# Performance work log

Hardware: AMD Instinct MI355X
Metric: run time of the kernel (lower is better)

## Reference

```python
import jax, jax.numpy as jnp
import numpy as np

N_LAYERS = 4
D_IN = 64
D_OUT = 64
D_MODEL = 512
D_STATE = 256
RMIN, RMAX, MAX_PHASE = 0.8, 0.95, 2.0 * np.pi


def setup_inputs() -> dict:
    key = jax.random.key(0)
    rng = np.random.default_rng(0)
    B, L = 8, 2048
    u = jax.random.normal(key, (B, L, D_IN), dtype=jnp.float32)
    # encoder/decoder (nn.Linear, bias=False): weight shape [out, in]
    encoder_w = jnp.asarray(rng.standard_normal((D_MODEL, D_IN)) / np.sqrt(D_IN), jnp.float32)
    decoder_w = jnp.asarray(rng.standard_normal((D_OUT, D_MODEL)) / np.sqrt(D_MODEL), jnp.float32)
    # LRU params per block (standard ring init on eigenvalues)
    u1 = rng.uniform(size=(N_LAYERS, D_STATE))
    u2 = rng.uniform(size=(N_LAYERS, D_STATE))
    nu_log = jnp.asarray(np.log(-0.5 * np.log(u1 * (RMAX**2 - RMIN**2) + RMIN**2)), jnp.float32)
    theta_log = jnp.asarray(np.log(MAX_PHASE * u2), jnp.float32)
    B_re = jnp.asarray(rng.standard_normal((N_LAYERS, D_STATE, D_MODEL)) / np.sqrt(2 * D_MODEL), jnp.float32)
    B_im = jnp.asarray(rng.standard_normal((N_LAYERS, D_STATE, D_MODEL)) / np.sqrt(2 * D_MODEL), jnp.float32)
    C_re = jnp.asarray(rng.standard_normal((N_LAYERS, D_MODEL, D_STATE)) / np.sqrt(D_STATE), jnp.float32)
    C_im = jnp.asarray(rng.standard_normal((N_LAYERS, D_MODEL, D_STATE)) / np.sqrt(D_STATE), jnp.float32)
    D = jnp.asarray(rng.standard_normal((N_LAYERS, D_MODEL)), jnp.float32)
    # GLU feedforward: y = (x W1^T) * sigmoid(x W2^T)
    W1 = jnp.asarray(rng.standard_normal((N_LAYERS, D_MODEL, D_MODEL)) / np.sqrt(D_MODEL), jnp.float32)
    W2 = jnp.asarray(rng.standard_normal((N_LAYERS, D_MODEL, D_MODEL)) / np.sqrt(D_MODEL), jnp.float32)
    res_logit = jnp.full((N_LAYERS,), -1.0, jnp.float32)
    return dict(u=u, encoder_w=encoder_w, decoder_w=decoder_w, nu_log=nu_log,
                theta_log=theta_log, B_re=B_re, B_im=B_im, C_re=C_re, C_im=C_im,
                D=D, W1=W1, W2=W2, res_logit=res_logit)


def _lru(x, nu, th, Bre, Bim, Cre, Cim, Dv):
    # diagonal complex LRU: h_t = lam*h_{t-1} + gamma*B u_t ; y = Re(C h) + D*u
    lam = jnp.exp(-jnp.exp(nu) + 1j * jnp.exp(th)).astype(jnp.complex64)  # [N]
    gam = jnp.sqrt(1.0 - jnp.abs(lam) ** 2).astype(jnp.complex64)
    Bc = (Bre + 1j * Bim).astype(jnp.complex64)  # [N, D]
    Bu = jnp.einsum('bld,nd->bln', x.astype(jnp.complex64), Bc) * gam  # [B,L,N]
    lam_b = jnp.broadcast_to(lam, Bu.shape)

    def comb(a, b):
        return (a[0] * b[0], a[1] * b[0] + b[1])

    _, h = jax.lax.associative_scan(comb, (lam_b, Bu), axis=1)
    Cc = (Cre + 1j * Cim).astype(jnp.complex64)  # [D, N]
    return jnp.real(jnp.einsum('bln,dn->bld', h, Cc)) + Dv * x


def reference(u, encoder_w, decoder_w, nu_log, theta_log, B_re, B_im, C_re, C_im, D, W1, W2, res_logit):
    x = jnp.einsum('bli,mi->blm', u, encoder_w)  # encoder
    for k in range(N_LAYERS):
        z = _lru(x, nu_log[k], theta_log[k], B_re[k], B_im[k], C_re[k], C_im[k], D[k])
        z = jnp.einsum('bld,od->blo', z, W1[k]) * jax.nn.sigmoid(jnp.einsum('bld,od->blo', z, W2[k]))
        x = x + jax.nn.sigmoid(res_logit[k]) * z  # gated residual (dropout=0)
    return jnp.einsum('blm,om->blo', x, decoder_w)  # decoder
```

## Files before the change

### kernel.cpp

```cpp
#include <hip/hip_runtime.h>
#include <cmath>

#define DM 512
#define DS 256
#define NL 4
#define BATCH 8
#define SEQ 2048
#define MROWS (BATCH*SEQ)
#define LCH 32
#define NCH 64

typedef unsigned short ushort_t;
typedef unsigned int uint_t;
typedef __attribute__((ext_vector_type(8))) short short8;
typedef __attribute__((ext_vector_type(4))) float floatx4;

__device__ __forceinline__ float sigmoidf_(float v) { return 1.0f / (1.0f + __expf(-v)); }

__device__ __forceinline__ ushort_t f2bf(float f) {
    union { float f; unsigned int u; } c; c.f = f;
    unsigned int u = c.u;
    u += 0x7fffu + ((u >> 16) & 1u);
    return (ushort_t)(u >> 16);
}
__device__ __forceinline__ float bf2f(uint_t h) {
    union { unsigned int u; float f; } c; c.u = (h & 0xffffu) << 16; return c.f;
}
__device__ __forceinline__ uint_t pack2(float a, float b) {
    return (uint_t)f2bf(a) | ((uint_t)f2bf(b) << 16);
}

#define AS1 __attribute__((address_space(1)))
#define AS3 __attribute__((address_space(3)))
__device__ __forceinline__ void gl_lds16(const void* g, void* l) {
    __builtin_amdgcn_global_load_lds((const AS1 uint_t*)g, (AS3 uint_t*)l, 16, 0, 0);
}

struct GemmArgs {
    const ushort_t* A;
    const ushort_t* Wa;
    const ushort_t* Wb;
    const ushort_t* xbf_in;
    const float* gam;
    const float* Dv;
    float* of32;
    ushort_t* obf;
    const float* resp;
    int K;
    int N;
    int layer;
};

#define PREFETCH_TILE(it_, buf_)                                                        \
    do {                                                                                \
        const size_t kb_ = (size_t)(it_) * 64;                                          \
        char* dst_ = smem + (buf_) * HALF;                                              \
        gl_lds16(Ap + (size_t)(wid * 16 + lrow) * Kb + kb_, dst_ + wid * 1024);         \
        gl_lds16(Ap + (size_t)((wid + 4) * 16 + lrow) * Kb + kb_,                       \
                 dst_ + (wid + 4) * 1024);                                              \
        gl_lds16(B0p + (size_t)(wid * 16 + lrow) * Kb + kb_, dst_ + AB + wid * 1024);   \
        if constexpr (BN == 128) {                                                      \
            gl_lds16(B0p + (size_t)((wid + 4) * 16 + lrow) * Kb + kb_,                  \
                     dst_ + AB + (wid + 4) * 1024);                                     \
        }                                                                               \
        if constexpr (DUAL) {                                                           \
            gl_lds16(B1p + (size_t)(wid * 16 + lrow) * Kb + kb_,                        \
                     dst_ + AB + BB + wid * 1024);                                      \
            if constexpr (BN == 128) {                                                  \
                gl_lds16(B1p + (size_t)((wid + 4) * 16 + lrow) * Kb + kb_,              \
                         dst_ + AB + BB + (wid + 4) * 1024);                            \
            }                                                                           \
        }                                                                               \
    } while (0)

template<int BN, int EPI, int DUAL>
__launch_bounds__(256, DUAL ? 2 : 3)
__global__ void mgemm(const GemmArgs p) {
    constexpr int BM = 128;
    constexpr int MT = (BN == 128) ? 4 : 2;
    constexpr int NT = 4;
    constexpr int WROWS = MT * 16;
    constexpr int AB = 8192;
    constexpr int BB = (BN == 128) ? 8192 : 4096;
    constexpr int B1B = DUAL ? BB : 0;
    constexpr int HALF = AB + BB + B1B;
    constexpr int EPB = (EPI == 4) ? 0 : 32 * 132 * 4;
    constexpr int SMB = (2 * HALF > EPB) ? 2 * HALF : EPB;
    __shared__ __align__(16) char smem[SMB];

    const int K = p.K, N = p.N;
    const int tid = threadIdx.x, lane = tid & 63, wid = tid >> 6;
    const int wm = (BN == 128) ? (wid & 1) : wid;
    const int wn = (BN == 128) ? (wid >> 1) : 0;
    const int m0 = blockIdx.x * BM, n0 = blockIdx.y * BN;
    const int q = lane >> 4, r16 = lane & 15;
    const int lrow = lane >> 2;
    const size_t Kb = (size_t)K * 2;
    const char* Ap  = (const char*)p.A  + (size_t)m0 * Kb + (lane & 3) * 16;
    const char* B0p = (const char*)p.Wa + (size_t)n0 * Kb + (lane & 3) * 16;
    const char* B1p = (const char*)p.Wb + (size_t)n0 * Kb + (lane & 3) * 16;

    floatx4 acc0[MT][NT] = {};
    floatx4 acc1[DUAL ? MT : 1][DUAL ? NT : 1] = {};

    const int iters = K >> 5;
    PREFETCH_TILE(0, 0);
    for (int it = 0; it < iters; ++it) {
        __syncthreads();
        if (it + 1 < iters) PREFETCH_TILE(it + 1, (it + 1) & 1);
        const ushort_t* As  = (const ushort_t*)(smem + (it & 1) * HALF);
        const ushort_t* Bs0 = (const ushort_t*)(smem + (it & 1) * HALF + AB);
        const ushort_t* Bs1 = (const ushort_t*)(smem + (it & 1) * HALF + AB + BB);

        short8 af[MT], b0[NT], b1[DUAL ? NT : 1];
#pragma unroll
        for (int i = 0; i < MT; ++i)
            af[i] = *(const short8*)&As[(wm * WROWS + i * 16 + r16) * 32 + q * 8];
#pragma unroll
        for (int j = 0; j < NT; ++j) {
            b0[j] = *(const short8*)&Bs0[(wn * 64 + j * 16 + r16) * 32 + q * 8];
            if constexpr (DUAL)
                b1[j] = *(const short8*)&Bs1[(wn * 64 + j * 16 + r16) * 32 + q * 8];
        }
#pragma unroll
        for (int i = 0; i < MT; ++i)
#pragma unroll
            for (int j = 0; j < NT; ++j) {
                acc0[i][j] = __builtin_amdgcn_mfma_f32_16x16x32_bf16(af[i], b0[j], acc0[i][j], 0, 0, 0);
                if constexpr (DUAL)
                    acc1[i][j] = __builtin_amdgcn_mfma_f32_16x16x32_bf16(af[i], b1[j], acc1[i][j], 0, 0, 0);
            }
    }

    if constexpr (EPI == 4) {
#pragma unroll
        for (int i = 0; i < MT; ++i)
#pragma unroll
            for (int j = 0; j < NT; ++j)
#pragma unroll
                for (int rr = 0; rr < 4; ++rr) {
                    const int row = m0 + wm * WROWS + i * 16 + q * 4 + rr;
                    const int col = wn * 64 + j * 16 + r16;
                    p.of32[(size_t)row * N + col] = acc0[i][j][rr];
                }
        return;
    } else {
        float* eps = (float*)smem;
        float rsv = 0.f;
        if constexpr (EPI == 3) rsv = sigmoidf_(p.resp[p.layer]);

#pragma unroll
        for (int i = 0; i < MT; ++i) {
            __syncthreads();
#pragma unroll
            for (int j = 0; j < NT; ++j) {
                const int colt = wn * 64 + j * 16 + r16;
#pragma unroll
                for (int rr = 0; rr < 4; ++rr) {
                    float v = acc0[i][j][rr];
                    if constexpr (EPI == 1) v *= p.gam[(n0 + colt) >> 1];
                    if constexpr (EPI == 3) v = rsv * v * sigmoidf_(acc1[i][j][rr]);
                    eps[(wm * 16 + q * 4 + rr) * 132 + colt] = v;
                }
            }
            __syncthreads();
            const int row_r = tid >> 3, colg = (tid & 7) * 16;
            const int grow = m0 + (row_r >> 4) * 64 + i * 16 + (row_r & 15);
            const int gcol = n0 + colg;
            float4 f[4];
#pragma unroll
            for (int c = 0; c < 4; ++c) f[c] = *(float4*)&eps[row_r * 132 + colg + c * 4];
            const size_t ob = (size_t)grow * N + gcol;

            if constexpr (EPI == 2) {
                uint_t xp[8];
                *(uint4*)(xp)     = *(const uint4*)(p.xbf_in + ob);
                *(uint4*)(xp + 4) = *(const uint4*)(p.xbf_in + ob + 8);
#pragma unroll
                for (int c = 0; c < 4; ++c) {
                    float4 dv = *(const float4*)(p.Dv + gcol + c * 4);
                    f[c].x += dv.x * bf2f(xp[2 * c]);
                    f[c].y += dv.y * bf2f(xp[2 * c] >> 16);
                    f[c].z += dv.z * bf2f(xp[2 * c + 1]);
                    f[c].w += dv.w * bf2f(xp[2 * c + 1] >> 16);
                }
            } else if constexpr (EPI == 3) {
                uint_t xp[8];
                *(uint4*)(xp)     = *(const uint4*)(p.xbf_in + ob);
                *(uint4*)(xp + 4) = *(const uint4*)(p.xbf_in + ob + 8);
#pragma unroll
                for (int c = 0; c < 4; ++c) {
                    f[c].x += bf2f(xp[2 * c]);
                    f[c].y += bf2f(xp[2 * c] >> 16);
                    f[c].z += bf2f(xp[2 * c + 1]);
                    f[c].w += bf2f(xp[2 * c + 1] >> 16);
                }
            }
            uint4 p0, p1;
            p0.x = pack2(f[0].x, f[0].y); p0.y = pack2(f[0].z, f[0].w);
            p0.z = pack2(f[1].x, f[1].y); p0.w = pack2(f[1].z, f[1].w);
            p1.x = pack2(f[2].x, f[2].y); p1.y = pack2(f[2].z, f[2].w);
            p1.z = pack2(f[3].x, f[3].y); p1.w = pack2(f[3].z, f[3].w);
            *(uint4*)(p.obf + ob) = p0;
            *(uint4*)(p.obf + ob + 8) = p1;
        }
    }
}

__global__ void prep_all(const float* __restrict__ u, const float* __restrict__ enc,
                         const float* __restrict__ dec, const float* __restrict__ nu,
                         const float* __restrict__ th,
                         const float* __restrict__ Bre, const float* __restrict__ Bim,
                         const float* __restrict__ Cre, const float* __restrict__ Cim,
                         const float* __restrict__ W1, const float* __restrict__ W2,
                         ushort_t* __restrict__ WBb, ushort_t* __restrict__ Wzb,
                         ushort_t* __restrict__ W1b, ushort_t* __restrict__ W2b,
                         ushort_t* __restrict__ encb, ushort_t* __restrict__ decb,
                         ushort_t* __restrict__ ubf,
                         float* __restrict__ lre, float* __restrict__ lim,
                         float* __restrict__ gm) {
    const int idx = blockIdx.x * 256 + threadIdx.x;
    const int k = idx & 511, n = (idx >> 9) & 511, l = idx >> 18;
    {
        const int s = n >> 1, part = n & 1;
        const float* src = part ? Bim : Bre;
        WBb[idx] = f2bf(src[((size_t)l * DS + s) * DM + k]);
    }
    {
        const int s = k >> 1, part = k & 1;
        float v = part ? -Cim[((size_t)l * DM + n) * DS + s]
                       :  Cre[((size_t)l * DM + n) * DS + s];
        Wzb[idx] = f2bf(v);
    }
    W1b[idx] = f2bf(W1[idx]);
    W2b[idx] = f2bf(W2[idx]);
    ubf[idx] = f2bf(u[idx]);
    if (idx < DM * 64) { encb[idx] = f2bf(enc[idx]); decb[idx] = f2bf(dec[idx]); }
    if (idx < NL * DS) {
        float a = expf(-expf(nu[idx])), t = expf(th[idx]);
        lre[idx] = a * cosf(t);
        lim[idx] = a * sinf(t);
        gm[idx] = sqrtf(fmaxf(0.f, 1.f - a * a));
    }
}

__global__ void scan_ends(const uint_t* __restrict__ Bu, const float* __restrict__ lre_,
                          const float* __restrict__ lim_, float* __restrict__ carry) {
    const int s = threadIdx.x;
    const int blk = blockIdx.x, b = blk >> 6, c = blk & 63;
    const float lre = lre_[s], lim = lim_[s];
    float hre = 0.f, him = 0.f;
    size_t base = ((size_t)b * SEQ + (size_t)c * LCH) * DS + s;
#pragma unroll 8
    for (int i = 0; i < LCH; ++i, base += DS) {
        uint_t u = Bu[base];
        float br = bf2f(u), bi = bf2f(u >> 16);
        float nr = fmaf(lre, hre, fmaf(-lim, him, br));
        float ni = fmaf(lre, him, fmaf(lim, hre, bi));
        hre = nr; him = ni;
    }
    carry[(size_t)blk * 512 + s] = hre;
    carry[(size_t)blk * 512 + DS + s] = him;
}

__global__ void scan_carry(float* __restrict__ carry, const float* __restrict__ lre_,
                           const float* __restrict__ lim_) {
    const int s = threadIdx.x, b = blockIdx.x;
    float pre = lre_[s], pim = lim_[s];
    for (int t = 0; t < 5; ++t) {
        float nr = pre * pre - pim * pim, ni = 2.f * pre * pim;
        pre = nr; pim = ni;
    }
    size_t base = (size_t)b * NCH * 512 + s;
    float gre = carry[base], gim = carry[base + DS];
    for (int c = 1; c < NCH; ++c) {
        size_t id = base + (size_t)c * 512;
        float cr = carry[id], ci = carry[id + DS];
        float nr = fmaf(pre, gre, fmaf(-pim, gim, cr));
        float ni = fmaf(pre, gim, fmaf(pim, gre, ci));
        gre = nr; gim = ni;
        carry[id] = gre; carry[id + DS] = gim;
    }
}

__global__ void scan_apply(const uint_t* __restrict__ Bu, const float* __restrict__ lre_,
                           const float* __restrict__ lim_, const float* __restrict__ carry,
                           uint_t* __restrict__ h) {
    const int s = threadIdx.x;
    const int blk = blockIdx.x, b = blk >> 6, c = blk & 63;
    const float lre = lre_[s], lim = lim_[s];
    float hre = 0.f, him = 0.f;
    if (c > 0) {
        size_t cb = (size_t)(blk - 1) * 512 + s;
        hre = carry[cb]; him = carry[cb + DS];
    }
    size_t base = ((size_t)b * SEQ + (size_t)c * LCH) * DS + s;
#pragma unroll 8
    for (int i = 0; i < LCH; ++i, base += DS) {
        uint_t u = Bu[base];
        float br = bf2f(u), bi = bf2f(u >> 16);
        float nr = fmaf(lre, hre, fmaf(-lim, him, br));
        float ni = fmaf(lre, him, fmaf(lim, hre, bi));
        hre = nr; him = ni;
        h[base] = pack2(hre, him);
    }
}

extern "C" void kernel_launch(void* const* d_in, const int* in_sizes, int n_in,
                              void* d_out, int out_size, void* d_ws, size_t ws_size,
                              hipStream_t stream) {
    const float* u   = (const float*)d_in[0];
    const float* enc = (const float*)d_in[1];
    const float* dec = (const float*)d_in[2];
    const float* nu  = (const float*)d_in[3];
    const float* th  = (const float*)d_in[4];
    const float* Bre = (const float*)d_in[5];
    const float* Bim = (const float*)d_in[6];
    const float* Cre = (const float*)d_in[7];
    const float* Cim = (const float*)d_in[8];
    const float* Dp  = (const float*)d_in[9];
    const float* W1  = (const float*)d_in[10];
    const float* W2  = (const float*)d_in[11];
    const float* res = (const float*)d_in[12];
    float* out = (float*)d_out;

    const size_t MD = (size_t)MROWS * DM;
    float* carry = (float*)d_ws;
    float* lre  = carry + (size_t)BATCH * NCH * 512;
    float* lim  = lre + NL * DS;
    float* gmt  = lim + NL * DS;
    ushort_t* xbf  = (ushort_t*)(gmt + NL * DS);
    ushort_t* Bubf = xbf + MD;
    ushort_t* hbf  = Bubf + MD;
    ushort_t* zbf  = hbf + MD;
    ushort_t* ubf  = zbf;
    ushort_t* WBb  = zbf + MD;
    ushort_t* Wzb  = WBb + (size_t)NL * DM * DM;
    ushort_t* W1b  = Wzb + (size_t)NL * DM * DM;
    ushort_t* W2b  = W1b + (size_t)NL * DM * DM;
    ushort_t* encb = W2b + (size_t)NL * DM * DM;
    ushort_t* decb = encb + DM * 64;

    prep_all<<<NL * DM * DM / 256, 256, 0, stream>>>(
        u, enc, dec, nu, th, Bre, Bim, Cre, Cim, W1, W2,
        WBb, Wzb, W1b, W2b, encb, decb, ubf, lre, lim, gmt);

    const dim3 gFull(MROWS / 128, DM / 128);

    {
        GemmArgs a = {};
        a.A = ubf; a.Wa = encb; a.K = 64; a.N = DM;
        a.obf = xbf;
        mgemm<128, 0, 0><<<gFull, 256, 0, stream>>>(a);
    }

    for (int k = 0; k < NL; ++k) {
        {
            GemmArgs a = {};
            a.A = xbf; a.Wa = WBb + (size_t)k * DM * DM; a.K = DM; a.N = DM;
            a.obf = Bubf; a.gam = gmt + k * DS;
            mgemm<128, 1, 0><<<gFull, 256, 0, stream>>>(a);
        }
        scan_ends<<<BATCH * NCH, 256, 0, stream>>>((const uint_t*)Bubf,
                                                   lre + k * DS, lim + k * DS, carry);
        scan_carry<<<BATCH, 256, 0, stream>>>(carry, lre + k * DS, lim + k * DS);
        scan_apply<<<BATCH * NCH, 256, 0, stream>>>((const uint_t*)Bubf,
                                                    lre + k * DS, lim + k * DS, carry,
                                                    (uint_t*)hbf);
        {
            GemmArgs a = {};
            a.A = hbf; a.Wa = Wzb + (size_t)k * DM * DM; a.K = DM; a.N = DM;
            a.obf = zbf; a.xbf_in = xbf; a.Dv = Dp + k * DM;
            mgemm<128, 2, 0><<<gFull, 256, 0, stream>>>(a);
        }
        {
            GemmArgs a = {};
            a.A = zbf; a.Wa = W1b + (size_t)k * DM * DM; a.Wb = W2b + (size_t)k * DM * DM;
            a.K = DM; a.N = DM;
            a.obf = xbf; a.xbf_in = xbf; a.resp = res; a.layer = k;
            mgemm<128, 3, 1><<<gFull, 256, 0, stream>>>(a);
        }
    }
    {
        GemmArgs a = {};
        a.A = xbf; a.Wa = decb; a.K = DM; a.N = 64;
        a.of32 = out;
        mgemm<64, 4, 0><<<dim3(MROWS / 128, 1), 256, 0, stream>>>(a);
    }
}
```

Before: 373.9 us.

## Fuse three-pass chunked scan into single-pass kernel with decoupled lookback

Replaces the scan_ends / scan_carry / scan_apply sequence with one kernel. Each block takes a ticket-ordered virtual block id, scans its chunk into registers, publishes its chunk-end state, and sets a per-batch bitmask flag. It then spin-waits on up to twelve preceding chunks and combines their end states with powers of lambda to get its prefix, which assumes contributions from farther chunks are negligible. This removes a second read of Bu, two kernel launches and the serial carry pass, in exchange for spin-wait synchronisation, higher register use and a truncated lookback approximation.

After: 764.2 us. 2.04x slower.

```diff
diff --git a/kernel.cpp b/kernel.cpp
--- a/kernel.cpp
+++ b/kernel.cpp
@@ -12,6 +12,7 @@
 
 typedef unsigned short ushort_t;
 typedef unsigned int uint_t;
+typedef unsigned long long ull_t;
 typedef __attribute__((ext_vector_type(8))) short short8;
 typedef __attribute__((ext_vector_type(4))) float floatx4;
 
@@ -218,7 +219,8 @@
                          ushort_t* __restrict__ encb, ushort_t* __restrict__ decb,
                          ushort_t* __restrict__ ubf,
                          float* __restrict__ lre, float* __restrict__ lim,
-                         float* __restrict__ gm) {
+                         float* __restrict__ gm,
+                         ull_t* __restrict__ msk, int* __restrict__ tkt) {
     const int idx = blockIdx.x * 256 + threadIdx.x;
     const int k = idx & 511, n = (idx >> 9) & 511, l = idx >> 18;
     {
@@ -242,68 +244,80 @@
         lim[idx] = a * sinf(t);
         gm[idx] = sqrtf(fmaxf(0.f, 1.f - a * a));
     }
-}
-
-__global__ void scan_ends(const uint_t* __restrict__ Bu, const float* __restrict__ lre_,
-                          const float* __restrict__ lim_, float* __restrict__ carry) {
+    if (idx < NL * BATCH) msk[idx] = 0ull;
+    if (idx < NL) tkt[idx] = 0;
+}
+
+__global__ __launch_bounds__(256) void scan_fused(
+        const uint_t* __restrict__ Bu, const float* __restrict__ lre_,
+        const float* __restrict__ lim_, float* __restrict__ carry,
+        ull_t* __restrict__ msk, int* __restrict__ tkt,
+        uint_t* __restrict__ h) {
+    __shared__ int vblk_s;
+    if (threadIdx.x == 0) vblk_s = atomicAdd(tkt, 1);
+    __syncthreads();
+    const int blk = vblk_s;
     const int s = threadIdx.x;
-    const int blk = blockIdx.x, b = blk >> 6, c = blk & 63;
+    const int b = blk >> 6, c = blk & 63;
     const float lre = lre_[s], lim = lim_[s];
-    float hre = 0.f, him = 0.f;
-    size_t base = ((size_t)b * SEQ + (size_t)c * LCH) * DS + s;
-#pragma unroll 8
-    for (int i = 0; i < LCH; ++i, base += DS) {
-        uint_t u = Bu[base];
-        float br = bf2f(u), bi = bf2f(u >> 16);
-        float nr = fmaf(lre, hre, fmaf(-lim, him, br));
-        float ni = fmaf(lre, him, fmaf(lim, hre, bi));
-        hre = nr; him = ni;
-    }
-    carry[(size_t)blk * 512 + s] = hre;
-    carry[(size_t)blk * 512 + DS + s] = him;
-}
-
-__global__ void scan_carry(float* __restrict__ carry, const float* __restrict__ lre_,
-                           const float* __restrict__ lim_) {
-    const int s = threadIdx.x, b = blockIdx.x;
-    float pre = lre_[s], pim = lim_[s];
-    for (int t = 0; t < 5; ++t) {
-        float nr = pre * pre - pim * pim, ni = 2.f * pre * pim;
-        pre = nr; pim = ni;
-    }
-    size_t base = (size_t)b * NCH * 512 + s;
-    float gre = carry[base], gim = carry[base + DS];
-    for (int c = 1; c < NCH; ++c) {
-        size_t id = base + (size_t)c * 512;
-        float cr = carry[id], ci = carry[id + DS];
-        float nr = fmaf(pre, gre, fmaf(-pim, gim, cr));
-        float ni = fmaf(pre, gim, fmaf(pim, gre, ci));
-        gre = nr; gim = ni;
-        carry[id] = gre; carry[id + DS] = gim;
-    }
-}
-
-__global__ void scan_apply(const uint_t* __restrict__ Bu, const float* __restrict__ lre_,
-                           const float* __restrict__ lim_, const float* __restrict__ carry,
-                           uint_t* __restrict__ h) {
-    const int s = threadIdx.x;
-    const int blk = blockIdx.x, b = blk >> 6, c = blk & 63;
-    const float lre = lre_[s], lim = lim_[s];
-    float hre = 0.f, him = 0.f;
+
+    float hre[LCH], him[LCH];
+    float xr = 0.f, xi = 0.f;
+    const size_t base = ((size_t)b * SEQ + (size_t)c * LCH) * DS + s;
+#pragma unroll
+    for (int i = 0; i < LCH; ++i) {
+        uint_t uu = Bu[base + (size_t)i * DS];
+        float br = bf2f(uu), bi = bf2f(uu >> 16);
+        float nr = fmaf(lre, xr, fmaf(-lim, xi, br));
+        float ni = fmaf(lre, xi, fmaf(lim, xr, bi));
+        xr = nr; xi = ni;
+        hre[i] = nr; him[i] = ni;
+    }
+
+    const size_t cb = (size_t)blk * 512 + s;
+    carry[cb] = xr; carry[cb + DS] = xi;
+    __syncthreads();
+    if (threadIdx.x == 0) {
+        __threadfence();
+        __hip_atomic_fetch_or(&msk[b], 1ull << c, __ATOMIC_RELEASE, __HIP_MEMORY_SCOPE_AGENT);
+    }
+
     if (c > 0) {
-        size_t cb = (size_t)(blk - 1) * 512 + s;
-        hre = carry[cb]; him = carry[cb + DS];
-    }
-    size_t base = ((size_t)b * SEQ + (size_t)c * LCH) * DS + s;
-#pragma unroll 8
-    for (int i = 0; i < LCH; ++i, base += DS) {
-        uint_t u = Bu[base];
-        float br = bf2f(u), bi = bf2f(u >> 16);
-        float nr = fmaf(lre, hre, fmaf(-lim, him, br));
-        float ni = fmaf(lre, him, fmaf(lim, hre, bi));
-        hre = nr; him = ni;
-        h[base] = pack2(hre, him);
-    }
+        float pre = lre, pim = lim;
+#pragma unroll
+        for (int t = 0; t < 5; ++t) {
+            float nr = pre * pre - pim * pim, ni = 2.f * pre * pim;
+            pre = nr; pim = ni;
+        }
+        const int depth = (c < 12) ? c : 12;
+        const ull_t need = ((1ull << depth) - 1ull) << (c - depth);
+        while ((__hip_atomic_load(&msk[b], __ATOMIC_ACQUIRE, __HIP_MEMORY_SCOPE_AGENT)
+                & need) != need) {
+            __builtin_amdgcn_s_sleep(2);
+        }
+        float gre = 0.f, gim = 0.f, pwr = 1.f, pwi = 0.f;
+        for (int j = c - 1; j >= c - depth; --j) {
+            const size_t jb = (size_t)(b * NCH + j) * 512 + s;
+            float er = carry[jb], ei = carry[jb + DS];
+            gre = fmaf(pwr, er, fmaf(-pwi, ei, gre));
+            gim = fmaf(pwr, ei, fmaf(pwi, er, gim));
+            float nr = pwr * pre - pwi * pim, ni = pwr * pim + pwi * pre;
+            pwr = nr; pwi = ni;
+        }
+        float pr = fmaf(lre, gre, -lim * gim);
+        float pi = fmaf(lre, gim,  lim * gre);
+#pragma unroll
+        for (int i = 0; i < LCH; ++i) {
+            hre[i] += pr; him[i] += pi;
+            float nr = fmaf(lre, pr, -lim * pi);
+            float ni = fmaf(lre, pi,  lim * pr);
+            pr = nr; pi = ni;
+        }
+    }
+
+#pragma unroll
+    for (int i = 0; i < LCH; ++i)
+        h[base + (size_t)i * DS] = pack2(hre[i], him[i]);
 }
 
 extern "C" void kernel_launch(void* const* d_in, const int* in_sizes, int n_in,
@@ -329,7 +343,9 @@
     float* lre  = carry + (size_t)BATCH * NCH * 512;
     float* lim  = lre + NL * DS;
     float* gmt  = lim + NL * DS;
-    ushort_t* xbf  = (ushort_t*)(gmt + NL * DS);
+    ull_t* msk  = (ull_t*)(gmt + NL * DS);
+    int*   tkt  = (int*)(msk + NL * BATCH);
+    ushort_t* xbf  = (ushort_t*)(tkt + NL);
     ushort_t* Bubf = xbf + MD;
     ushort_t* hbf  = Bubf + MD;
     ushort_t* zbf  = hbf + MD;
@@ -343,7 +359,7 @@
 
     prep_all<<<NL * DM * DM / 256, 256, 0, stream>>>(
         u, enc, dec, nu, th, Bre, Bim, Cre, Cim, W1, W2,
-        WBb, Wzb, W1b, W2b, encb, decb, ubf, lre, lim, gmt);
+        WBb, Wzb, W1b, W2b, encb, decb, ubf, lre, lim, gmt, msk, tkt);
 
     const dim3 gFull(MROWS / 128, DM / 128);
 
@@ -361,12 +377,9 @@
             a.obf = Bubf; a.gam = gmt + k * DS;
             mgemm<128, 1, 0><<<gFull, 256, 0, stream>>>(a);
         }
-        scan_ends<<<BATCH * NCH, 256, 0, stream>>>((const uint_t*)Bubf,
-                                                   lre + k * DS, lim + k * DS, carry);
-        scan_carry<<<BATCH, 256, 0, stream>>>(carry, lre + k * DS, lim + k * DS);
-        scan_apply<<<BATCH * NCH, 256, 0, stream>>>((const uint_t*)Bubf,
-                                                    lre + k * DS, lim + k * DS, carry,
-                                                    (uint_t*)hbf);
+        scan_fused<<<BATCH * NCH, 256, 0, stream>>>(
+            (const uint_t*)Bubf, lre + k * DS, lim + k * DS, carry,
+            msk + (size_t)k * BATCH, tkt + k, (uint_t*)hbf);
         {
             GemmArgs a = {};
             a.A = hbf; a.Wa = Wzb + (size_t)k * DM * DM; a.K = DM; a.N = DM;
```

## Replace serial scan carry kernel with truncated lookback and remap GEMM blocks per XCD

Applied to the files above, without the earlier changes.

Drops the scan_carry kernel, which walks the 64 chunk carries one after another with only 8 blocks. Instead, each scan_apply block builds its incoming state from up to 12 preceding chunk end-states, weighted by powers of lambda^32. This removes a launch and a serial, low-occupancy pass, at the cost of a small truncation error that depends on |lambda| staying bounded below 1 (it is at most 0.95 by construction). Separately, the GEMM remaps block indices so that blocks sharing an XCD handle contiguous M tiles, which is meant to improve L2 reuse. The remap hardcodes a grid width of 128.

After: 388.5 us. +3.9%, slower.

```diff
diff --git a/kernel.cpp b/kernel.cpp
--- a/kernel.cpp
+++ b/kernel.cpp
@@ -92,7 +92,13 @@
     const int tid = threadIdx.x, lane = tid & 63, wid = tid >> 6;
     const int wm = (BN == 128) ? (wid & 1) : wid;
     const int wn = (BN == 128) ? (wid >> 1) : 0;
-    const int m0 = blockIdx.x * BM, n0 = blockIdx.y * BN;
+
+    const int flat = blockIdx.y * 128 + blockIdx.x;
+    const int xcd = flat & 7, sidx = flat >> 3;
+    const int bx = xcd * 16 + (sidx & 15);
+    const int by = sidx >> 4;
+
+    const int m0 = bx * BM, n0 = by * BN;
     const int q = lane >> 4, r16 = lane & 15;
     const int lrow = lane >> 2;
     const size_t Kb = (size_t)K * 2;
@@ -244,8 +250,9 @@
     }
 }
 
-__global__ void scan_ends(const uint_t* __restrict__ Bu, const float* __restrict__ lre_,
-                          const float* __restrict__ lim_, float* __restrict__ carry) {
+__global__ __launch_bounds__(256) void scan_ends(
+        const uint_t* __restrict__ Bu, const float* __restrict__ lre_,
+        const float* __restrict__ lim_, float* __restrict__ carry) {
     const int s = threadIdx.x;
     const int blk = blockIdx.x, b = blk >> 6, c = blk & 63;
     const float lre = lre_[s], lim = lim_[s];
@@ -263,46 +270,44 @@
     carry[(size_t)blk * 512 + DS + s] = him;
 }
 
-__global__ void scan_carry(float* __restrict__ carry, const float* __restrict__ lre_,
-                           const float* __restrict__ lim_) {
-    const int s = threadIdx.x, b = blockIdx.x;
-    float pre = lre_[s], pim = lim_[s];
-    for (int t = 0; t < 5; ++t) {
-        float nr = pre * pre - pim * pim, ni = 2.f * pre * pim;
-        pre = nr; pim = ni;
-    }
-    size_t base = (size_t)b * NCH * 512 + s;
-    float gre = carry[base], gim = carry[base + DS];
-    for (int c = 1; c < NCH; ++c) {
-        size_t id = base + (size_t)c * 512;
-        float cr = carry[id], ci = carry[id + DS];
-        float nr = fmaf(pre, gre, fmaf(-pim, gim, cr));
-        float ni = fmaf(pre, gim, fmaf(pim, gre, ci));
-        gre = nr; gim = ni;
-        carry[id] = gre; carry[id + DS] = gim;
-    }
-}
-
-__global__ void scan_apply(const uint_t* __restrict__ Bu, const float* __restrict__ lre_,
-                           const float* __restrict__ lim_, const float* __restrict__ carry,
-                           uint_t* __restrict__ h) {
+__global__ __launch_bounds__(256) void scan_apply_lb(
+        const uint_t* __restrict__ Bu, const float* __restrict__ lre_,
+        const float* __restrict__ lim_, const float* __restrict__ carry,
+        uint_t* __restrict__ h) {
     const int s = threadIdx.x;
     const int blk = blockIdx.x, b = blk >> 6, c = blk & 63;
     const float lre = lre_[s], lim = lim_[s];
-    float hre = 0.f, him = 0.f;
+
+    float gre = 0.f, gim = 0.f;
     if (c > 0) {
-        size_t cb = (size_t)(blk - 1) * 512 + s;
-        hre = carry[cb]; him = carry[cb + DS];
-    }
+        float are = lre, aim = lim;
+#pragma unroll
+        for (int t = 0; t < 5; ++t) {
+            float nr = are * are - aim * aim, ni = 2.f * are * aim;
+            are = nr; aim = ni;
+        }
+        const int depth = (c < 12) ? c : 12;
+        float pwr = 1.f, pwi = 0.f;
+        for (int j = c - 1; j >= c - depth; --j) {
+            const size_t jb = (size_t)(b * NCH + j) * 512 + s;
+            float er = carry[jb], ei = carry[jb + DS];
+            gre = fmaf(pwr, er, fmaf(-pwi, ei, gre));
+            gim = fmaf(pwr, ei, fmaf(pwi, er, gim));
+            float nr = pwr * are - pwi * aim, ni = pwr * aim + pwi * are;
+            pwr = nr; pwi = ni;
+        }
+    }
+
+    float hr = gre, hi = gim;
     size_t base = ((size_t)b * SEQ + (size_t)c * LCH) * DS + s;
 #pragma unroll 8
     for (int i = 0; i < LCH; ++i, base += DS) {
-        uint_t u = Bu[base];
-        float br = bf2f(u), bi = bf2f(u >> 16);
-        float nr = fmaf(lre, hre, fmaf(-lim, him, br));
-        float ni = fmaf(lre, him, fmaf(lim, hre, bi));
-        hre = nr; him = ni;
-        h[base] = pack2(hre, him);
+        uint_t uu = Bu[base];
+        float br = bf2f(uu), bi = bf2f(uu >> 16);
+        float nr = fmaf(lre, hr, fmaf(-lim, hi, br));
+        float ni = fmaf(lre, hi, fmaf(lim, hr, bi));
+        hr = nr; hi = ni;
+        h[base] = pack2(hr, hi);
     }
 }
 
@@ -363,10 +368,9 @@
         }
         scan_ends<<<BATCH * NCH, 256, 0, stream>>>((const uint_t*)Bubf,
                                                    lre + k * DS, lim + k * DS, carry);
-        scan_carry<<<BATCH, 256, 0, stream>>>(carry, lre + k * DS, lim + k * DS);
-        scan_apply<<<BATCH * NCH, 256, 0, stream>>>((const uint_t*)Bubf,
-                                                    lre + k * DS, lim + k * DS, carry,
-                                                    (uint_t*)hbf);
+        scan_apply_lb<<<BATCH * NCH, 256, 0, stream>>>((const uint_t*)Bubf,
+                                                       lre + k * DS, lim + k * DS, carry,
+                                                       (uint_t*)hbf);
         {
             GemmArgs a = {};
             a.A = hbf; a.Wa = Wzb + (size_t)k * DM * DM; a.K = DM; a.N = DM;
```
